# Performance work log

Hardware: AMD Instinct MI355X
Metric: run time of the kernel (lower is better)

Reference implementation:

```python
import jax, jax.numpy as jnp
import numpy as np

L = 5        # n_layers
H = 8        # heads
DH = 32      # dim_head = n_hidden // heads
D = 256      # n_hidden
KR = 4       # key_ratio
QKD = KR * DH  # 128, q/k feature dim
IN = 3       # fun_dim + space_dim
OUT = 1      # out_dim
N = 32768    # number of mesh points
EPS = 1e-5

def _ln(x, g, b):
    m = jnp.mean(x, axis=-1, keepdims=True)
    v = jnp.var(x, axis=-1, keepdims=True)
    return (x - m) * jax.lax.rsqrt(v + EPS) * g + b

def _gelu(x):
    return jax.nn.gelu(x, approximate=False)  # torch nn.GELU default (erf)

def setup_inputs() -> dict:
    key = jax.random.key(0)
    ks = iter(jax.random.split(key, 64))
    def w(*s):
        return jax.random.normal(next(ks), s, jnp.float32) * 0.02
    return {
        "x": jax.random.normal(next(ks), (N, IN), jnp.float32),
        # preprocess MLP: Linear(IN,2D)+GELU, Linear(2D,D)
        "pre_w1": w(IN, 2 * D), "pre_b1": jnp.zeros((2 * D,), jnp.float32),
        "pre_w2": w(2 * D, D), "pre_b2": jnp.zeros((D,), jnp.float32),
        "placeholder": jax.random.uniform(next(ks), (D,), jnp.float32) / D,
        # per-block params stacked over L
        "ln1_g": jnp.ones((L, D), jnp.float32), "ln1_b": jnp.zeros((L, D), jnp.float32),
        "inp_w": w(L, D, D), "inp_b": jnp.zeros((L, D), jnp.float32),
        "temp_q": jnp.full((L, H), 0.5, jnp.float32), "temp_k": jnp.full((L, H), 0.5, jnp.float32),
        "wq": w(L, DH, QKD), "wk": w(L, DH, QKD), "wv": w(L, DH, DH),
        "out_w1": w(L, D, D), "out_b1": jnp.zeros((L, D), jnp.float32),
        "out_w2": w(L, D, D), "out_b2": jnp.zeros((L, D), jnp.float32),
        "ln2_g": jnp.ones((L, D), jnp.float32), "ln2_b": jnp.zeros((L, D), jnp.float32),
        "mlp_w1": w(L, D, D), "mlp_b1": jnp.zeros((L, D), jnp.float32),  # mlp_ratio=1 -> hidden=D
        "mlp_w2": w(L, D, D), "mlp_b2": jnp.zeros((L, D), jnp.float32),
        # last-layer head
        "ln3_g": jnp.ones((D,), jnp.float32), "ln3_b": jnp.zeros((D,), jnp.float32),
        "head_w": w(D, OUT), "head_b": jnp.zeros((OUT,), jnp.float32),
    }

def reference(x, pre_w1, pre_b1, pre_w2, pre_b2, placeholder,
              ln1_g, ln1_b, inp_w, inp_b, temp_q, temp_k, wq, wk, wv,
              out_w1, out_b1, out_w2, out_b2, ln2_g, ln2_b,
              mlp_w1, mlp_b1, mlp_w2, mlp_b2, ln3_g, ln3_b, head_w, head_b):
    # preprocess + placeholder bias
    fx = _gelu(x[None] @ pre_w1 + pre_b1) @ pre_w2 + pre_b2  # [1, N, D]
    fx = fx + placeholder
    for i in range(L):
        # --- LinearNO attention block ---
        h = _ln(fx, ln1_g[i], ln1_b[i])
        xm = h @ inp_w[i] + inp_b[i]                       # [1, N, D]
        xm = xm.reshape(1, N, H, DH).transpose(0, 2, 1, 3)  # [1, H, N, DH]
        q = jnp.einsum('bhnd,de->bhne', xm, wq[i])          # [1, H, N, QKD]
        k = jnp.einsum('bhnd,de->bhne', xm, wk[i])          # [1, H, N, QKD]
        v = jnp.einsum('bhnd,dc->bhnc', xm, wv[i])          # [1, H, N, DH]
        tq = jnp.clip(temp_q[i], 0.1, 2.0)[None, :, None, None]
        tk = jnp.clip(temp_k[i], 0.1, 2.0)[None, :, None, None]
        q = jax.nn.softmax(q / tq, axis=-1)  # over feature dim
        k = jax.nn.softmax(k / tk, axis=-2)  # over point dim
        kv = jnp.einsum('bhnd,bhnc->bhdc', k, v)    # [1, H, QKD, DH]
        qkv = jnp.einsum('bhnd,bhdc->bhnc', q, kv)  # [1, H, N, DH]
        qkv = qkv.transpose(0, 2, 1, 3).reshape(1, N, D)
        attn = _gelu(qkv @ out_w1[i] + out_b1[i]) @ out_w2[i] + out_b2[i]
        fx = attn + fx
        # --- MLP block (n_layers=0, res=False: pre + post only) ---
        h2 = _ln(fx, ln2_g[i], ln2_b[i])
        fx = _gelu(h2 @ mlp_w1[i] + mlp_b1[i]) @ mlp_w2[i] + mlp_b2[i] + fx
    # last block head: mlp2(ln_3(fx))
    out = _ln(fx, ln3_g, ln3_b) @ head_w + head_b  # [1, N, OUT]
    return out[0]  # module returns fx[0]
```

## Files before the change

### kernel.cpp

```cpp
#include <hip/hip_runtime.h>
#include <hip/hip_bf16.h>
#include <math.h>

constexpr int NP  = 32768;
constexpr int HH  = 8;

typedef short bf16x8 __attribute__((ext_vector_type(8)));
typedef float f32x4  __attribute__((ext_vector_type(4)));

__device__ __forceinline__ float gelu_f(float x) {
    return 0.5f * x * (1.0f + erff(x * 0.70710678118654752f));
}

__device__ __forceinline__ unsigned short f2bf(float x) {
    union { float f; unsigned u; } v; v.f = x;
    unsigned r = v.u + 0x7fffu + ((v.u >> 16) & 1u);
    return (unsigned short)(r >> 16);
}

__device__ __forceinline__ float bf2f(unsigned short h) {
    union { unsigned u; float f; } v; v.u = ((unsigned)h) << 16;
    return v.f;
}

__global__ __launch_bounds__(256) void transpose_bf16_k(
    const float* __restrict__ src, unsigned short* __restrict__ dst, int K)
{
    __shared__ float tile[32][33];
    int g = blockIdx.z;
    int k0 = blockIdx.x * 32, c0 = blockIdx.y * 32;
    int tx = threadIdx.x & 31, ty = threadIdx.x >> 5;
    const float* s = src + (size_t)g * K * 256;
    unsigned short* d = dst + (size_t)g * 256 * K;
    #pragma unroll
    for (int rr = 0; rr < 4; ++rr) {
        int r = ty + rr * 8;
        tile[r][tx] = s[(size_t)(k0 + r) * 256 + c0 + tx];
    }
    __syncthreads();
    #pragma unroll
    for (int rr = 0; rr < 4; ++rr) {
        int r = ty + rr * 8;
        d[(size_t)(c0 + r) * K + k0 + tx] = f2bf(tile[tx][r]);
    }
}

__global__ __launch_bounds__(256) void transpose_scale_bf16_k(
    const float* __restrict__ src, const float* __restrict__ g,
    unsigned short* __restrict__ dst, int K)
{
    __shared__ float tile[32][33];
    int z = blockIdx.z;
    int k0 = blockIdx.x * 32, c0 = blockIdx.y * 32;
    int tx = threadIdx.x & 31, ty = threadIdx.x >> 5;
    const float* s = src + (size_t)z * K * 256;
    unsigned short* d = dst + (size_t)z * 256 * K;
    #pragma unroll
    for (int rr = 0; rr < 4; ++rr) {
        int r = ty + rr * 8;
        tile[r][tx] = s[(size_t)(k0 + r) * 256 + c0 + tx];
    }
    __syncthreads();
    float gs = g[z * 256 + k0 + tx];
    #pragma unroll
    for (int rr = 0; rr < 4; ++rr) {
        int r = ty + rr * 8;
        d[(size_t)(c0 + r) * K + k0 + tx] = f2bf(gs * tile[tx][r]);
    }
}

__global__ __launch_bounds__(256) void colsum_k(
    const float* __restrict__ W, const float* __restrict__ g,
    const float* __restrict__ b, float* __restrict__ c2, float* __restrict__ c1)
{
    int z = blockIdx.z, c = threadIdx.x;
    const float* Wz = W + (size_t)z * 65536;
    const float* gz = g + z * 256;
    const float* bz = b + z * 256;
    float s2 = 0.f, s1 = 0.f;
    for (int k = 0; k < 256; ++k) {
        float w = Wz[k * 256 + c];
        s2 += gz[k] * w;
        s1 += bz[k] * w;
    }
    c2[z * 256 + c] = s2;
    c1[z * 256 + c] = s1;
}

__global__ __launch_bounds__(256) void prep_wkvT(
    const float* __restrict__ wk, const float* __restrict__ wv,
    const float* __restrict__ wq,
    unsigned short* __restrict__ wkT, unsigned short* __restrict__ wvT,
    unsigned short* __restrict__ wqT)
{
    int l = blockIdx.x, tid = threadIdx.x;
    for (int idx = tid; idx < 4096; idx += 256) {
        int d = idx >> 5, k = idx & 31;
        wkT[l * 4096 + idx] = f2bf(wk[l * 4096 + k * 128 + d]);
        wqT[l * 4096 + idx] = f2bf(wq[l * 4096 + k * 128 + d]);
    }
    for (int idx = tid; idx < 1024; idx += 256) {
        int c = idx >> 5, k = idx & 31;
        wvT[l * 1024 + idx] = f2bf(wv[l * 1024 + k * 32 + c]);
    }
}

template<bool GENA, bool AF32, bool LNFOLD, bool DOGELU, bool RESID, bool STATS, bool PERM>
__global__ __launch_bounds__(256) void gemm_bf(
    const unsigned short* __restrict__ Ah, const float* __restrict__ Af,
    const unsigned short* __restrict__ Wt,
    const float* __restrict__ bias, const float* __restrict__ bias2,
    float* __restrict__ outF, unsigned short* __restrict__ outH,
    const float* __restrict__ stats_in, float* __restrict__ stats_out,
    const float* __restrict__ c1v, const float* __restrict__ c2vec,
    const float* __restrict__ genx, const float* __restrict__ genw1,
    const float* __restrict__ genb1, int K)
{
    __shared__ __align__(16) unsigned short As[128 * 64];
    __shared__ __align__(16) unsigned short Bs[128 * 64];
    __shared__ float rmean[LNFOLD ? 128 : 1];
    __shared__ float rrstd[LNFOLD ? 128 : 1];
    __shared__ float w1s[GENA ? 1536 : 1];
    __shared__ float b1s[GENA ? 512 : 1];
    __shared__ float x3s[GENA ? 512 : 1];

    const int tid = threadIdx.x;
    const int rBase = blockIdx.x * 128, cBase = blockIdx.y * 128;

    if constexpr (GENA) {
        for (int i2 = tid; i2 < 1536; i2 += 256) w1s[i2] = genw1[i2];
        for (int i2 = tid; i2 < 512; i2 += 256) b1s[i2] = genb1[i2];
        if (tid < 128) {
            x3s[tid * 4 + 0] = genx[(size_t)(rBase + tid) * 3 + 0];
            x3s[tid * 4 + 1] = genx[(size_t)(rBase + tid) * 3 + 1];
            x3s[tid * 4 + 2] = genx[(size_t)(rBase + tid) * 3 + 2];
        }
        __syncthreads();
    }
    if constexpr (LNFOLD) {
        if (tid < 128) {
            const float* sp = stats_in + (size_t)(rBase + tid) * 8;
            float4 s0 = *(const float4*)sp;
            float4 s1 = *(const float4*)(sp + 4);
            float mean = (s0.x + s0.z + s1.x + s1.z) * (1.f / 256.f);
            float ex2  = (s0.y + s0.w + s1.y + s1.w) * (1.f / 256.f);
            rmean[tid] = mean;
            rrstd[tid] = rsqrtf(fmaxf(ex2 - mean * mean, 0.f) + 1e-5f);
        }
        __syncthreads();
    }

    f32x4 acc[4][4];
    #pragma unroll
    for (int i = 0; i < 4; ++i)
        #pragma unroll
        for (int j = 0; j < 4; ++j)
            acc[i][j] = (f32x4){0.f, 0.f, 0.f, 0.f};

    const int lane = tid & 63, wid = tid >> 6;
    const int wr = wid >> 1, wc = wid & 1;
    const int lrow = lane & 15, quad = lane >> 4;
    const int srow = tid >> 3;
    const int sch  = tid & 7;

    for (int kc = 0; kc < K; kc += 64) {
        if constexpr (GENA) {
            #pragma unroll
            for (int it = 0; it < 4; ++it) {
                int row = srow + it * 32;
                float x0 = x3s[row * 4 + 0], x1 = x3s[row * 4 + 1], x2 = x3s[row * 4 + 2];
                unsigned short pk[8];
                #pragma unroll
                for (int j = 0; j < 8; ++j) {
                    int k = kc + sch * 8 + j;
                    float t = x0 * w1s[k] + x1 * w1s[512 + k] + x2 * w1s[1024 + k] + b1s[k];
                    pk[j] = f2bf(gelu_f(t));
                }
                *(uint4*)&As[row * 64 + ((sch ^ (row & 7)) << 3)] = *(uint4*)pk;
            }
        } else if constexpr (AF32) {
            #pragma unroll
            for (int it = 0; it < 4; ++it) {
                int row = srow + it * 32;
                const float* ap = Af + (size_t)(rBase + row) * K + kc + sch * 8;
                float4 a0 = *(const float4*)ap;
                float4 a1 = *(const float4*)(ap + 4);
                unsigned short pk[8];
                pk[0] = f2bf(a0.x); pk[1] = f2bf(a0.y); pk[2] = f2bf(a0.z); pk[3] = f2bf(a0.w);
                pk[4] = f2bf(a1.x); pk[5] = f2bf(a1.y); pk[6] = f2bf(a1.z); pk[7] = f2bf(a1.w);
                *(uint4*)&As[row * 64 + ((sch ^ (row & 7)) << 3)] = *(uint4*)pk;
            }
        } else {
            #pragma unroll
            for (int it = 0; it < 4; ++it) {
                int row = srow + it * 32;
                uint4 av = *(const uint4*)(Ah + (size_t)(rBase + row) * K + kc + sch * 8);
                *(uint4*)&As[row * 64 + ((sch ^ (row & 7)) << 3)] = av;
            }
        }
        #pragma unroll
        for (int it = 0; it < 4; ++it) {
            int n = srow + it * 32;
            uint4 wv_ = *(const uint4*)(Wt + (size_t)(cBase + n) * K + kc + sch * 8);
            *(uint4*)&Bs[n * 64 + ((sch ^ (n & 7)) << 3)] = wv_;
        }
        __syncthreads();
        #pragma unroll
        for (int ks = 0; ks < 2; ++ks) {
            bf16x8 af[4], bfr[4];
            #pragma unroll
            for (int t = 0; t < 4; ++t) {
                int row = wr * 64 + t * 16 + lrow;
                af[t] = *(bf16x8*)&As[row * 64 + (((ks * 4 + quad) ^ (row & 7)) << 3)];
                int n = wc * 64 + t * 16 + lrow;
                bfr[t] = *(bf16x8*)&Bs[n * 64 + (((ks * 4 + quad) ^ (n & 7)) << 3)];
            }
            #pragma unroll
            for (int ti = 0; ti < 4; ++ti)
                #pragma unroll
                for (int tj = 0; tj < 4; ++tj)
                    acc[ti][tj] = __builtin_amdgcn_mfma_f32_16x16x32_bf16(
                        af[ti], bfr[tj], acc[ti][tj], 0, 0, 0);
        }
        __syncthreads();
    }

    float c1b[4], c2r[4];
    #pragma unroll
    for (int tj = 0; tj < 4; ++tj) {
        int gcol = cBase + wc * 64 + tj * 16 + lrow;
        float b = bias[gcol];
        if (bias2) b += bias2[gcol];
        if constexpr (LNFOLD) {
            c1b[tj] = c1v[gcol] + b;
            c2r[tj] = c2vec[gcol];
        } else {
            c1b[tj] = b;
            c2r[tj] = 0.f;
        }
    }
    #pragma unroll
    for (int ti = 0; ti < 4; ++ti) {
        #pragma unroll
        for (int r = 0; r < 4; ++r) {
            int rib = wr * 64 + ti * 16 + quad * 4 + r;
            int grow = rBase + rib;
            float mean = 0.f, rstd = 1.f;
            if constexpr (LNFOLD) { mean = rmean[rib]; rstd = rrstd[rib]; }
            float vv[4];
            #pragma unroll
            for (int tj = 0; tj < 4; ++tj) {
                float t = acc[ti][tj][r];
                float v;
                if constexpr (LNFOLD) v = rstd * (t - mean * c2r[tj]) + c1b[tj];
                else                  v = t + c1b[tj];
                if constexpr (DOGELU) v = gelu_f(v);
                vv[tj] = v;
            }
            if constexpr (RESID) {
                #pragma unroll
                for (int tj = 0; tj < 4; ++tj) {
                    int gcol = cBase + wc * 64 + tj * 16 + lrow;
                    vv[tj] += outF[(size_t)grow * 256 + gcol];
                }
            }
            if constexpr (STATS) {
                float rs = vv[0] + vv[1] + vv[2] + vv[3];
                float rq = vv[0]*vv[0] + vv[1]*vv[1] + vv[2]*vv[2] + vv[3]*vv[3];
                #pragma unroll
                for (int m = 1; m < 16; m <<= 1) {
                    rs += __shfl_xor(rs, m);
                    rq += __shfl_xor(rq, m);
                }
                if (lrow == 0) {
                    stats_out[(size_t)grow * 8 + (blockIdx.y * 2 + wc) * 2 + 0] = rs;
                    stats_out[(size_t)grow * 8 + (blockIdx.y * 2 + wc) * 2 + 1] = rq;
                }
            }
            #pragma unroll
            for (int tj = 0; tj < 4; ++tj) {
                int gcol = cBase + wc * 64 + tj * 16 + lrow;
                if constexpr (PERM) {
                    size_t pidx = (size_t)(gcol >> 5) * NP * 32 + (size_t)grow * 32 + (gcol & 31);
                    if (outF) outF[pidx] = vv[tj];
                    if (outH) outH[pidx] = f2bf(vv[tj]);
                } else {
                    if (outF) outF[(size_t)grow * 256 + gcol] = vv[tj];
                    if (outH) outH[(size_t)grow * 256 + gcol] = f2bf(vv[tj]);
                }
            }
        }
    }
}

__global__ __launch_bounds__(256) void kv6_kernel(
    const unsigned short* __restrict__ xm2h, const unsigned short* __restrict__ wkT,
    const unsigned short* __restrict__ wvT, const float* __restrict__ tk_arr,
    float* __restrict__ partials, int layer)
{
    __shared__ __align__(16) unsigned short xs[64 * 32];
    __shared__ __align__(16) unsigned short wks[128 * 32];
    __shared__ __align__(16) unsigned short wvs[32 * 32];
    __shared__ __align__(16) unsigned short els[128 * 72];
    __shared__ __align__(16) unsigned short vls[32 * 72];
    __shared__ float sums[4 * 128];

    const int tid = threadIdx.x;
    const int h = blockIdx.y;
    const int rowBase = blockIdx.x * 512;
    const int w = tid >> 6, lane = tid & 63;
    const int lrow = lane & 15, quad = lane >> 4;

    float tk = fminf(fmaxf(tk_arr[layer * 8 + h], 0.1f), 2.0f);
    float invtk = 1.0f / tk;

    #pragma unroll
    for (int it = 0; it < 2; ++it) {
        int cid = tid + it * 256;
        int d = cid >> 2, kc = cid & 3;
        uint4 v = *(const uint4*)(wkT + d * 32 + kc * 8);
        *(uint4*)&wks[d * 32 + ((kc ^ (d & 3)) << 3)] = v;
    }
    if (tid < 128) {
        int c = tid >> 2, kc = tid & 3;
        uint4 v = *(const uint4*)(wvT + c * 32 + kc * 8);
        *(uint4*)&wvs[c * 32 + ((kc ^ (c & 3)) << 3)] = v;
    }

    f32x4 acc2[2][2];
    #pragma unroll
    for (int di = 0; di < 2; ++di)
        #pragma unroll
        for (int ci = 0; ci < 2; ++ci)
            acc2[di][ci] = (f32x4){0.f, 0.f, 0.f, 0.f};
    float seacc[8];
    #pragma unroll
    for (int dt = 0; dt < 8; ++dt) seacc[dt] = 0.f;

    const unsigned short* src = xm2h + (size_t)h * NP * 32 + (size_t)rowBase * 32;

    for (int sub = 0; sub < 8; ++sub) {
        __syncthreads();
        {
            int row = tid >> 2, kc = tid & 3;
            uint4 v = *(const uint4*)(src + (size_t)(sub * 64 + row) * 32 + kc * 8);
            *(uint4*)&xs[row * 32 + ((kc ^ (row & 3)) << 3)] = v;
        }
        __syncthreads();
        int arow = w * 16 + lrow;
        bf16x8 ax = *(bf16x8*)&xs[arow * 32 + ((quad ^ (arow & 3)) << 3)];
        #pragma unroll
        for (int ct = 0; ct < 2; ++ct) {
            int c = ct * 16 + lrow;
            bf16x8 bw = *(bf16x8*)&wvs[c * 32 + ((quad ^ (c & 3)) << 3)];
            f32x4 cc = (f32x4){0.f, 0.f, 0.f, 0.f};
            cc = __builtin_amdgcn_mfma_f32_16x16x32_bf16(ax, bw, cc, 0, 0, 0);
            unsigned short pk[4];
            pk[0] = f2bf(cc[0]); pk[1] = f2bf(cc[1]);
            pk[2] = f2bf(cc[2]); pk[3] = f2bf(cc[3]);
            *(uint2*)&vls[(ct * 16 + lrow) * 72 + w * 16 + quad * 4] = *(uint2*)pk;
        }
        #pragma unroll
        for (int dt = 0; dt < 8; ++dt) {
            int d = dt * 16 + lrow;
            bf16x8 bw = *(bf16x8*)&wks[d * 32 + ((quad ^ (d & 3)) << 3)];
            f32x4 cc = (f32x4){0.f, 0.f, 0.f, 0.f};
            cc = __builtin_amdgcn_mfma_f32_16x16x32_bf16(ax, bw, cc, 0, 0, 0);
            unsigned short pk[4];
            float se = 0.f;
            #pragma unroll
            for (int r = 0; r < 4; ++r) {
                float l = fminf(fmaxf(cc[r] * invtk, -30.f), 30.f);
                unsigned short eb = f2bf(__expf(l));
                pk[r] = eb;
                se += bf2f(eb);
            }
            seacc[dt] += se;
            *(uint2*)&els[d * 72 + w * 16 + quad * 4] = *(uint2*)pk;
        }
        __syncthreads();
        #pragma unroll
        for (int di = 0; di < 2; ++di) {
            int dm = (2 * w + di) * 16 + lrow;
            #pragma unroll
            for (int ks = 0; ks < 2; ++ks) {
                bf16x8 ae = *(bf16x8*)&els[dm * 72 + ks * 32 + quad * 8];
                #pragma unroll
                for (int ci = 0; ci < 2; ++ci) {
                    int cn = ci * 16 + lrow;
                    bf16x8 bv = *(bf16x8*)&vls[cn * 72 + ks * 32 + quad * 8];
                    acc2[di][ci] = __builtin_amdgcn_mfma_f32_16x16x32_bf16(
                        ae, bv, acc2[di][ci], 0, 0, 0);
                }
            }
        }
    }

    float* outp = partials + ((size_t)h * 64 + blockIdx.x) * 4224;
    #pragma unroll
    for (int di = 0; di < 2; ++di)
        #pragma unroll
        for (int ci = 0; ci < 2; ++ci)
            #pragma unroll
            for (int r = 0; r < 4; ++r) {
                int d = (2 * w + di) * 16 + quad * 4 + r;
                int c = ci * 16 + lrow;
                outp[d * 32 + c] = acc2[di][ci][r];
            }
    #pragma unroll
    for (int dt = 0; dt < 8; ++dt) {
        float s = seacc[dt];
        s += __shfl_xor(s, 16);
        s += __shfl_xor(s, 32);
        if (quad == 0) sums[w * 128 + dt * 16 + lrow] = s;
    }
    __syncthreads();
    if (tid < 128)
        outp[4096 + tid] = sums[tid] + sums[128 + tid] + sums[256 + tid] + sums[384 + tid];
}

__global__ __launch_bounds__(256) void kv_reduce_kernel(
    const float* __restrict__ partials, unsigned short* __restrict__ kvT,
    float* __restrict__ sumexp)
{
    int gid = blockIdx.x * 256 + threadIdx.x;
    if (gid >= 8 * 4224) return;
    int h = gid / 4224, idx = gid % 4224;
    const float* base = partials + (size_t)h * 64 * 4224 + idx;
    float s = 0.f;
    #pragma unroll 8
    for (int c = 0; c < 64; ++c) s += base[(size_t)c * 4224];
    if (idx < 4096) {
        int d = idx >> 5, c = idx & 31;
        kvT[(size_t)h * 4096 + c * 128 + d] = f2bf(s);
    } else {
        sumexp[h * 128 + (idx - 4096)] = s;
    }
}

__global__ __launch_bounds__(256) void qkv6_kernel(
    const unsigned short* __restrict__ xm2h, const unsigned short* __restrict__ wqT,
    const float* __restrict__ tq_arr, const unsigned short* __restrict__ kvT,
    const float* __restrict__ sumexp, float* __restrict__ outD, int layer)
{
    __shared__ __align__(16) unsigned short xs[64 * 32];
    __shared__ __align__(16) unsigned short wqs[128 * 32];
    __shared__ __align__(16) unsigned short kvb[32 * 136];
    __shared__ __align__(16) unsigned short els[64 * 136];
    __shared__ float ises[128];

    const int tid = threadIdx.x;
    const int h = blockIdx.y;
    const int rowBase = blockIdx.x * 64;
    const int w = tid >> 6, lane = tid & 63;
    const int lrow = lane & 15, quad = lane >> 4;

    float tq = fminf(fmaxf(tq_arr[layer * 8 + h], 0.1f), 2.0f);
    float invtq = 1.0f / tq;

    if (tid < 128) ises[tid] = 1.0f / sumexp[h * 128 + tid];
    #pragma unroll
    for (int it = 0; it < 2; ++it) {
        int cid = tid + it * 256;
        int d = cid >> 2, kc = cid & 3;
        uint4 v = *(const uint4*)(wqT + d * 32 + kc * 8);
        *(uint4*)&wqs[d * 32 + ((kc ^ (d & 3)) << 3)] = v;
    }
    #pragma unroll
    for (int it = 0; it < 2; ++it) {
        int cid = tid + it * 256;
        int c = cid >> 4, k8 = cid & 15;
        uint4 v = *(const uint4*)(kvT + (size_t)h * 4096 + c * 128 + k8 * 8);
        *(uint4*)&kvb[c * 136 + k8 * 8] = v;
    }
    {
        int row = tid >> 2, kc = tid & 3;
        uint4 v = *(const uint4*)(xm2h + (size_t)h * NP * 32 +
                                  (size_t)(rowBase + row) * 32 + kc * 8);
        *(uint4*)&xs[row * 32 + ((kc ^ (row & 3)) << 3)] = v;
    }
    __syncthreads();

    int arow = w * 16 + lrow;
    bf16x8 ax = *(bf16x8*)&xs[arow * 32 + ((quad ^ (arow & 3)) << 3)];
    f32x4 lg[8];
    #pragma unroll
    for (int dt = 0; dt < 8; ++dt) {
        int d = dt * 16 + lrow;
        bf16x8 bw = *(bf16x8*)&wqs[d * 32 + ((quad ^ (d & 3)) << 3)];
        f32x4 cc = (f32x4){0.f, 0.f, 0.f, 0.f};
        lg[dt] = __builtin_amdgcn_mfma_f32_16x16x32_bf16(ax, bw, cc, 0, 0, 0);
    }
    float isv[8];
    #pragma unroll
    for (int dt = 0; dt < 8; ++dt) isv[dt] = ises[dt * 16 + lrow];

    #pragma unroll
    for (int r = 0; r < 4; ++r) {
        float m = lg[0][r];
        #pragma unroll
        for (int dt = 1; dt < 8; ++dt) m = fmaxf(m, lg[dt][r]);
        m = fmaxf(m, __shfl_xor(m, 1));
        m = fmaxf(m, __shfl_xor(m, 2));
        m = fmaxf(m, __shfl_xor(m, 4));
        m = fmaxf(m, __shfl_xor(m, 8));
        float e[8], s = 0.f;
        #pragma unroll
        for (int dt = 0; dt < 8; ++dt) {
            e[dt] = __expf((lg[dt][r] - m) * invtq);
            s += e[dt];
        }
        s += __shfl_xor(s, 1);
        s += __shfl_xor(s, 2);
        s += __shfl_xor(s, 4);
        s += __shfl_xor(s, 8);
        float inv = 1.0f / s;
        int erow = w * 16 + quad * 4 + r;
        #pragma unroll
        for (int dt = 0; dt < 8; ++dt)
            els[erow * 136 + dt * 16 + lrow] = f2bf(e[dt] * inv * isv[dt]);
    }

    #pragma unroll
    for (int ct = 0; ct < 2; ++ct) {
        f32x4 oc = (f32x4){0.f, 0.f, 0.f, 0.f};
        #pragma unroll
        for (int ks = 0; ks < 4; ++ks) {
            bf16x8 ae = *(bf16x8*)&els[(w * 16 + lrow) * 136 + ks * 32 + quad * 8];
            bf16x8 bv = *(bf16x8*)&kvb[(ct * 16 + lrow) * 136 + ks * 32 + quad * 8];
            oc = __builtin_amdgcn_mfma_f32_16x16x32_bf16(ae, bv, oc, 0, 0, 0);
        }
        #pragma unroll
        for (int r = 0; r < 4; ++r)
            outD[(size_t)(rowBase + w * 16 + quad * 4 + r) * 256 +
                 h * 32 + ct * 16 + lrow] = oc[r];
    }
}

__global__ __launch_bounds__(256) void head_kernel(
    const float* __restrict__ fx, const float* __restrict__ g, const float* __restrict__ b,
    const float* __restrict__ hw, const float* __restrict__ hb, float* __restrict__ out)
{
    int lane = threadIdx.x & 63;
    int row = blockIdx.x * 4 + (threadIdx.x >> 6);
    float4 v = *(const float4*)(fx + (size_t)row * 256 + lane * 4);
    float s1 = v.x + v.y + v.z + v.w;
    float s2 = v.x * v.x + v.y * v.y + v.z * v.z + v.w * v.w;
    #pragma unroll
    for (int m = 1; m < 64; m <<= 1) { s1 += __shfl_xor(s1, m); s2 += __shfl_xor(s2, m); }
    float mean = s1 * 0.00390625f;
    float rstd = rsqrtf(fmaxf(s2 * 0.00390625f - mean * mean, 0.f) + 1e-5f);
    float4 gg = *(const float4*)(g + lane * 4);
    float4 bb = *(const float4*)(b + lane * 4);
    float4 w4 = *(const float4*)(hw + lane * 4);
    float d = ((v.x - mean) * rstd * gg.x + bb.x) * w4.x
            + ((v.y - mean) * rstd * gg.y + bb.y) * w4.y
            + ((v.z - mean) * rstd * gg.z + bb.z) * w4.z
            + ((v.w - mean) * rstd * gg.w + bb.w) * w4.w;
    #pragma unroll
    for (int m = 1; m < 64; m <<= 1) d += __shfl_xor(d, m);
    if (lane == 0) out[row] = d + hb[0];
}

extern "C" void kernel_launch(void* const* d_in, const int* in_sizes, int n_in,
                              void* d_out, int out_size, void* d_ws, size_t ws_size,
                              hipStream_t stream)
{
    const float* x      = (const float*)d_in[0];
    const float* pre_w1 = (const float*)d_in[1];
    const float* pre_b1 = (const float*)d_in[2];
    const float* pre_w2 = (const float*)d_in[3];
    const float* pre_b2 = (const float*)d_in[4];
    const float* ph     = (const float*)d_in[5];
    const float* ln1_g  = (const float*)d_in[6];
    const float* ln1_b  = (const float*)d_in[7];
    const float* inp_w  = (const float*)d_in[8];
    const float* inp_b  = (const float*)d_in[9];
    const float* temp_q = (const float*)d_in[10];
    const float* temp_k = (const float*)d_in[11];
    const float* wq     = (const float*)d_in[12];
    const float* wk     = (const float*)d_in[13];
    const float* wv     = (const float*)d_in[14];
    const float* out_w1 = (const float*)d_in[15];
    const float* out_b1 = (const float*)d_in[16];
    const float* out_w2 = (const float*)d_in[17];
    const float* out_b2 = (const float*)d_in[18];
    const float* ln2_g  = (const float*)d_in[19];
    const float* ln2_b  = (const float*)d_in[20];
    const float* mlp_w1 = (const float*)d_in[21];
    const float* mlp_b1 = (const float*)d_in[22];
    const float* mlp_w2 = (const float*)d_in[23];
    const float* mlp_b2 = (const float*)d_in[24];
    const float* ln3_g  = (const float*)d_in[25];
    const float* ln3_b  = (const float*)d_in[26];
    const float* head_w = (const float*)d_in[27];
    const float* head_b = (const float*)d_in[28];
    float* out = (float*)d_out;

    float* fx = (float*)d_ws;
    unsigned short* fxh = (unsigned short*)(fx + (size_t)NP * 256);
    unsigned short* ChH = fxh + (size_t)NP * 256;
    unsigned short* xm2h = ChH;
    float* scr = (float*)(ChH + (size_t)NP * 256);
    float* st = scr + (size_t)NP * 256;
    unsigned short* kvT = (unsigned short*)(st + (size_t)NP * 8);
    float* se = (float*)(kvT + 8 * 4096);
    float* c1i = se + 8 * 128;
    float* c2i = c1i + 1280;
    float* c1m = c2i + 1280;
    float* c2m = c1m + 1280;
    unsigned short* wtPre = (unsigned short*)(c2m + 1280);
    unsigned short* wtL   = wtPre + 256 * 512;
    unsigned short* wkT   = wtL + 25 * 65536;
    unsigned short* wvT   = wkT + 5 * 4096;
    unsigned short* wqT   = wvT + 5 * 1024;

    unsigned short* wtIn = wtL;
    unsigned short* wtO1 = wtL +  5 * 65536;
    unsigned short* wtO2 = wtL + 10 * 65536;
    unsigned short* wtM1 = wtL + 15 * 65536;
    unsigned short* wtM2 = wtL + 20 * 65536;

    dim3 bt(256);

    transpose_bf16_k<<<dim3(16, 8, 1), bt, 0, stream>>>(pre_w2, wtPre, 512);
    transpose_scale_bf16_k<<<dim3(8, 8, 5), bt, 0, stream>>>(inp_w,  ln1_g, wtIn, 256);
    transpose_bf16_k<<<dim3(8, 8, 5), bt, 0, stream>>>(out_w1, wtO1, 256);
    transpose_bf16_k<<<dim3(8, 8, 5), bt, 0, stream>>>(out_w2, wtO2, 256);
    transpose_scale_bf16_k<<<dim3(8, 8, 5), bt, 0, stream>>>(mlp_w1, ln2_g, wtM1, 256);
    transpose_bf16_k<<<dim3(8, 8, 5), bt, 0, stream>>>(mlp_w2, wtM2, 256);
    colsum_k<<<dim3(1, 1, 5), bt, 0, stream>>>(inp_w,  ln1_g, ln1_b, c2i, c1i);
    colsum_k<<<dim3(1, 1, 5), bt, 0, stream>>>(mlp_w1, ln2_g, ln2_b, c2m, c1m);
    prep_wkvT<<<dim3(5), bt, 0, stream>>>(wk, wv, wq, wkT, wvT, wqT);

    dim3 gg(256, 2);

    gemm_bf<true, false, false, false, false, true, false><<<gg, bt, 0, stream>>>(
        nullptr, nullptr, wtPre, pre_b2, ph, fx, fxh, nullptr, st,
        nullptr, nullptr, x, pre_w1, pre_b1, 512);

    for (int i = 0; i < 5; ++i) {
        gemm_bf<false, false, true, false, false, false, true><<<gg, bt, 0, stream>>>(
            fxh, nullptr, wtIn + (size_t)i * 65536, inp_b + i * 256, nullptr, nullptr, xm2h,
            st, nullptr, c1i + i * 256, c2i + i * 256, nullptr, nullptr, nullptr, 256);
        kv6_kernel<<<dim3(64, 8), bt, 0, stream>>>(
            xm2h, wkT + (size_t)i * 4096, wvT + (size_t)i * 1024, temp_k, scr, i);
        kv_reduce_kernel<<<dim3(132), bt, 0, stream>>>(scr, kvT, se);
        qkv6_kernel<<<dim3(512, 8), bt, 0, stream>>>(
            xm2h, wqT + (size_t)i * 4096, temp_q, kvT, se, scr, i);
        gemm_bf<false, true, false, true, false, false, false><<<gg, bt, 0, stream>>>(
            nullptr, scr, wtO1 + (size_t)i * 65536, out_b1 + i * 256, nullptr,
            nullptr, ChH, nullptr, nullptr, nullptr, nullptr, nullptr, nullptr, nullptr, 256);
        gemm_bf<false, false, false, false, true, true, false><<<gg, bt, 0, stream>>>(
            ChH, nullptr, wtO2 + (size_t)i * 65536, out_b2 + i * 256, nullptr, fx, fxh,
            nullptr, st, nullptr, nullptr, nullptr, nullptr, nullptr, 256);
        gemm_bf<false, false, true, true, false, false, false><<<gg, bt, 0, stream>>>(
            fxh, nullptr, wtM1 + (size_t)i * 65536, mlp_b1 + i * 256, nullptr, scr, nullptr,
            st, nullptr, c1m + i * 256, c2m + i * 256, nullptr, nullptr, nullptr, 256);
        gemm_bf<false, true, false, false, true, true, false><<<gg, bt, 0, stream>>>(
            nullptr, scr, wtM2 + (size_t)i * 65536, mlp_b2 + i * 256, nullptr, fx, fxh,
            nullptr, st, nullptr, nullptr, nullptr, nullptr, nullptr, 256);
    }
    head_kernel<<<dim3(NP / 4), bt, 0, stream>>>(fx, ln3_g, ln3_b, head_w, head_b, out);
}
```

Measured before the change: 971.8 us.

## Store attention/MLP intermediates as bf16 and read fp32 fx directly in LN GEMMs

The qkv kernel and the MLP first GEMM now write bf16 intermediates instead of fp32, so the downstream GEMMs read bf16 A operands and move half the bytes. The residual GEMMs no longer emit a separate bf16 copy of fx. The LN-fused GEMMs instead read the fp32 fx directly and convert it on load. This trades the extra fxh write for a heavier fp32 read in two GEMMs, and adds rounding on the attention output.

New measurement: 1.325 ms. 36.4% more time.

```diff
diff --git a/kernel.cpp b/kernel.cpp
--- a/kernel.cpp
+++ b/kernel.cpp
@@ -441,7 +441,7 @@
 __global__ __launch_bounds__(256) void qkv6_kernel(
     const unsigned short* __restrict__ xm2h, const unsigned short* __restrict__ wqT,
     const float* __restrict__ tq_arr, const unsigned short* __restrict__ kvT,
-    const float* __restrict__ sumexp, float* __restrict__ outD, int layer)
+    const float* __restrict__ sumexp, unsigned short* __restrict__ outH, int layer)
 {
     __shared__ __align__(16) unsigned short xs[64 * 32];
     __shared__ __align__(16) unsigned short wqs[128 * 32];
@@ -532,8 +532,8 @@
         }
         #pragma unroll
         for (int r = 0; r < 4; ++r)
-            outD[(size_t)(rowBase + w * 16 + quad * 4 + r) * 256 +
-                 h * 32 + ct * 16 + lrow] = oc[r];
+            outH[(size_t)(rowBase + w * 16 + quad * 4 + r) * 256 +
+                 h * 32 + ct * 16 + lrow] = f2bf(oc[r]);
     }
 }
 
@@ -621,6 +621,9 @@
     unsigned short* wtM1 = wtL + 15 * 65536;
     unsigned short* wtM2 = wtL + 20 * 65536;
 
+    unsigned short* qh = (unsigned short*)scr;
+    unsigned short* mh = (unsigned short*)scr;
+
     dim3 bt(256);
 
     transpose_bf16_k<<<dim3(16, 8, 1), bt, 0, stream>>>(pre_w2, wtPre, 512);
@@ -636,29 +639,29 @@
     dim3 gg(256, 2);
 
     gemm_bf<true, false, false, false, false, true, false><<<gg, bt, 0, stream>>>(
-        nullptr, nullptr, wtPre, pre_b2, ph, fx, fxh, nullptr, st,
+        nullptr, nullptr, wtPre, pre_b2, ph, fx, nullptr, nullptr, st,
         nullptr, nullptr, x, pre_w1, pre_b1, 512);
 
     for (int i = 0; i < 5; ++i) {
-        gemm_bf<false, false, true, false, false, false, true><<<gg, bt, 0, stream>>>(
-            fxh, nullptr, wtIn + (size_t)i * 65536, inp_b + i * 256, nullptr, nullptr, xm2h,
+        gemm_bf<false, true, true, false, false, false, true><<<gg, bt, 0, stream>>>(
+            nullptr, fx, wtIn + (size_t)i * 65536, inp_b + i * 256, nullptr, nullptr, xm2h,
             st, nullptr, c1i + i * 256, c2i + i * 256, nullptr, nullptr, nullptr, 256);
         kv6_kernel<<<dim3(64, 8), bt, 0, stream>>>(
             xm2h, wkT + (size_t)i * 4096, wvT + (size_t)i * 1024, temp_k, scr, i);
         kv_reduce_kernel<<<dim3(132), bt, 0, stream>>>(scr, kvT, se);
         qkv6_kernel<<<dim3(512, 8), bt, 0, stream>>>(
-            xm2h, wqT + (size_t)i * 4096, temp_q, kvT, se, scr, i);
-        gemm_bf<false, true, false, true, false, false, false><<<gg, bt, 0, stream>>>(
-            nullptr, scr, wtO1 + (size_t)i * 65536, out_b1 + i * 256, nullptr,
+            xm2h, wqT + (size_t)i * 4096, temp_q, kvT, se, qh, i);
+        gemm_bf<false, false, false, true, false, false, false><<<gg, bt, 0, stream>>>(
+            qh, nullptr, wtO1 + (size_t)i * 65536, out_b1 + i * 256, nullptr,
             nullptr, ChH, nullptr, nullptr, nullptr, nullptr, nullptr, nullptr, nullptr, 256);
         gemm_bf<false, false, false, false, true, true, false><<<gg, bt, 0, stream>>>(
-            ChH, nullptr, wtO2 + (size_t)i * 65536, out_b2 + i * 256, nullptr, fx, fxh,
+            ChH, nullptr, wtO2 + (size_t)i * 65536, out_b2 + i * 256, nullptr, fx, nullptr,
             nullptr, st, nullptr, nullptr, nullptr, nullptr, nullptr, 256);
-        gemm_bf<false, false, true, true, false, false, false><<<gg, bt, 0, stream>>>(
-            fxh, nullptr, wtM1 + (size_t)i * 65536, mlp_b1 + i * 256, nullptr, scr, nullptr,
+        gemm_bf<false, true, true, true, false, false, false><<<gg, bt, 0, stream>>>(
+            nullptr, fx, wtM1 + (size_t)i * 65536, mlp_b1 + i * 256, nullptr, nullptr, mh,
             st, nullptr, c1m + i * 256, c2m + i * 256, nullptr, nullptr, nullptr, 256);
-        gemm_bf<false, true, false, false, true, true, false><<<gg, bt, 0, stream>>>(
-            nullptr, scr, wtM2 + (size_t)i * 65536, mlp_b2 + i * 256, nullptr, fx, fxh,
+        gemm_bf<false, false, false, false, true, true, false><<<gg, bt, 0, stream>>>(
+            mh, nullptr, wtM2 + (size_t)i * 65536, mlp_b2 + i * 256, nullptr, fx, nullptr,
             nullptr, st, nullptr, nullptr, nullptr, nullptr, nullptr, 256);
     }
     head_kernel<<<dim3(NP / 4), bt, 0, stream>>>(fx, ln3_g, ln3_b, head_w, head_b, out);
```
